# Kernel tuning notes

Measured on AMD Instinct MI355X. Metric: run time of the kernel, lower is better.

## Reference

```python
import jax, jax.numpy as jnp
import numpy as np

B = 64            # number of graphs
N = 2048          # nodes per graph (equal segments; torch.stack in the original requires this)
D = 256           # hidden_dim
G = 4             # num_groups
SUBS = 3          # subclasses per group -> num_classes = 12
C = G * SUBS


def _layer_norm(x, g, b, eps=1e-5):
    mu = jnp.mean(x, axis=-1, keepdims=True)
    var = jnp.var(x, axis=-1, keepdims=True)
    return (x - mu) * jax.lax.rsqrt(var + eps) * g + b


def setup_inputs() -> dict:
    key = jax.random.key(0)
    ks = jax.random.split(key, 20)
    T = B * N
    inp = {
        "node_features": jax.random.normal(ks[0], (T, D), dtype=jnp.float32),
        "batch": jnp.repeat(jnp.arange(B, dtype=jnp.int64), N),  # sorted, equal-size segments
        # group queries (nn.Parameter randn)
        "group_queries": jax.random.normal(ks[1], (G, D), dtype=jnp.float32),
        # per-group projector MLP: D -> 2D -> SUBS*D (stacked over groups)
        "proj_w1": jax.random.normal(ks[2], (G, D, 2 * D), dtype=jnp.float32) * (1.0 / np.sqrt(D)),
        "proj_b1": jnp.zeros((G, 2 * D), dtype=jnp.float32),
        "proj_w2": jax.random.normal(ks[3], (G, 2 * D, SUBS * D), dtype=jnp.float32) * (1.0 / np.sqrt(2 * D)),
        "proj_b2": jnp.zeros((G, SUBS * D), dtype=jnp.float32),
        # output_proj_12: LN -> Linear(D, D//2) -> ReLU -> Linear(D//2, 1)
        "ln12_g": jnp.ones((D,), dtype=jnp.float32),
        "ln12_b": jnp.zeros((D,), dtype=jnp.float32),
        "w12a": jax.random.normal(ks[4], (D, D // 2), dtype=jnp.float32) * (1.0 / np.sqrt(D)),
        "b12a": jnp.zeros((D // 2,), dtype=jnp.float32),
        "w12b": jax.random.normal(ks[5], (D // 2, 1), dtype=jnp.float32) * (1.0 / np.sqrt(D // 2)),
        "b12b": jnp.zeros((1,), dtype=jnp.float32),
        # output_proj_4
        "ln4_g": jnp.ones((D,), dtype=jnp.float32),
        "ln4_b": jnp.zeros((D,), dtype=jnp.float32),
        "w4a": jax.random.normal(ks[6], (D, D // 2), dtype=jnp.float32) * (1.0 / np.sqrt(D)),
        "b4a": jnp.zeros((D // 2,), dtype=jnp.float32),
        "w4b": jax.random.normal(ks[7], (D // 2, 1), dtype=jnp.float32) * (1.0 / np.sqrt(D // 2)),
        "b4b": jnp.zeros((1,), dtype=jnp.float32),
    }
    return inp


def reference(node_features, batch, group_queries, proj_w1, proj_b1, proj_w2, proj_b2,
              ln12_g, ln12_b, w12a, b12a, w12b, b12b,
              ln4_g, ln4_b, w4a, b4a, w4b, b4b):
    # --- derive class queries from group queries (per-group MLP) ---
    h = jax.nn.relu(jnp.einsum('gd,gdh->gh', group_queries, proj_w1) + proj_b1)   # [G, 2D]
    flat = jnp.einsum('gh,ghk->gk', h, proj_w2) + proj_b2                         # [G, SUBS*D]
    # group g maps to global class indices [3g, 3g+1, 3g+2] -> simple reshape gives ordered queries
    class_queries = flat.reshape(C, D)                                            # [12, D]

    scale = jnp.asarray(D ** 0.5, node_features.dtype)
    # equal-size sorted segments: reshape total nodes into [B, N, D] per-graph blocks
    nodes = node_features.reshape(B, N, D)

    # --- 12-class attention pooling ---
    scores12 = jnp.einsum('cd,bnd->bcn', class_queries, nodes) / scale            # [B, 12, N]
    attn12 = jax.nn.softmax(scores12, axis=-1)
    pooled12 = jnp.einsum('bcn,bnd->bcd', attn12, nodes)                          # [B, 12, D]
    x12 = _layer_norm(pooled12, ln12_g, ln12_b)
    logits_12 = (jax.nn.relu(x12 @ w12a + b12a) @ w12b + b12b)[..., 0]            # [B, 12]

    # --- 4-group attention pooling ---
    scores4 = jnp.einsum('gd,bnd->bgn', group_queries, nodes) / scale             # [B, 4, N]
    attn4 = jax.nn.softmax(scores4, axis=-1)
    pooled4 = jnp.einsum('bgn,bnd->bgd', attn4, nodes)                            # [B, 4, D]
    x4 = _layer_norm(pooled4, ln4_g, ln4_b)
    logits_4 = (jax.nn.relu(x4 @ w4a + b4a) @ w4b + b4b)[..., 0]                  # [B, 4]

    return (logits_12, logits_4, attn12)
```

## Files before the change

### kernel.cpp

```cpp
#include <hip/hip_runtime.h>
#include <math.h>

#define BG   64
#define NN   2048
#define DD   256
#define CQ   16
#define NCH  8

static constexpr size_t WS_Q16 = 0;
static constexpr size_t WS_H   = 4096;
static constexpr size_t WS_S   = 6144;
static constexpr size_t WS_ML  = WS_S + (size_t)BG * CQ * NN;
static constexpr size_t WS_PL  = WS_ML + (size_t)BG * NCH * 32;
static constexpr size_t WS_FML = WS_PL + (size_t)BG * NCH * CQ * DD;
static constexpr size_t WS_FIL = WS_FML + 1024;

__global__ __launch_bounds__(256) void kA1(const float* __restrict__ gq,
                                           const float* __restrict__ w1,
                                           const float* __restrict__ b1,
                                           float* __restrict__ ws) {
    int blk = blockIdx.x;
    int g   = blk >> 4;
    int jb  = (blk & 15) * 32;
    int t   = threadIdx.x;
    __shared__ float qlds[256];
    qlds[t] = gq[g * 256 + t];
    if ((blk & 15) == 0) ws[WS_Q16 + (12 + g) * 256 + t] = gq[g * 256 + t];
    __syncthreads();
    int jl = t & 31, dp = t >> 5;
    float acc = 0.f;
    const float* wp = w1 + ((size_t)g * 256) * 512 + jb + jl;
    #pragma unroll 8
    for (int i = 0; i < 32; ++i) {
        int d = dp * 32 + i;
        acc += qlds[d] * wp[(size_t)d * 512];
    }
    __shared__ float red[8][33];
    red[dp][jl] = acc;
    __syncthreads();
    if (dp == 0) {
        float s = 0.f;
        #pragma unroll
        for (int p = 0; p < 8; ++p) s += red[p][jl];
        s += b1[g * 512 + jb + jl];
        ws[WS_H + g * 512 + jb + jl] = fmaxf(s, 0.f);
    }
}

__global__ __launch_bounds__(256) void kA2(const float* __restrict__ w2,
                                           const float* __restrict__ b2,
                                           float* __restrict__ ws) {
    int blk = blockIdx.x;
    int g   = blk / 48;
    int kb  = (blk % 48) * 16;
    int t   = threadIdx.x;
    __shared__ float hlds[512];
    hlds[t]       = ws[WS_H + g * 512 + t];
    hlds[t + 256] = ws[WS_H + g * 512 + t + 256];
    __syncthreads();
    int kl = t & 15, dp = t >> 4;
    float acc = 0.f;
    const float* wp = w2 + ((size_t)g * 512) * 768 + kb + kl;
    #pragma unroll 8
    for (int i = 0; i < 32; ++i) {
        int jj = dp * 32 + i;
        acc += hlds[jj] * wp[(size_t)jj * 768];
    }
    __shared__ float red[16][17];
    red[dp][kl] = acc;
    __syncthreads();
    if (dp == 0) {
        float s = 0.f;
        #pragma unroll
        for (int p = 0; p < 16; ++p) s += red[p][kl];
        ws[WS_Q16 + g * 768 + kb + kl] = s + b2[g * 768 + kb + kl];
    }
}

__global__ __launch_bounds__(256) void kF(const float* __restrict__ x,
                                          float* __restrict__ ws) {
    __shared__ float4 qlds[CQ * 64];
    __shared__ float  wlds[CQ * 256];
    __shared__ float  mbuf[CQ], lbuf[CQ];

    int t   = threadIdx.x;
    int blk = blockIdx.x;
    int b   = blk >> 3, ch = blk & 7;
    int gn0 = b * NN + ch * 256;

    const float4* qg = (const float4*)(ws + WS_Q16);
    #pragma unroll
    for (int i = 0; i < 4; ++i) qlds[t + i * 256] = qg[t + i * 256];
    __syncthreads();

    const float4* xa = (const float4*)x + (size_t)(gn0 + t) * 64;
    float sc[CQ];
    #pragma unroll
    for (int c = 0; c < CQ; ++c) sc[c] = 0.f;

    float4 buf[8];
    #pragma unroll
    for (int i = 0; i < 8; ++i) buf[i] = xa[i];
    for (int base = 0; base < 64; base += 8) {
        float4 cur[8];
        #pragma unroll
        for (int i = 0; i < 8; ++i) cur[i] = buf[i];
        if (base + 8 < 64) {
            #pragma unroll
            for (int i = 0; i < 8; ++i) buf[i] = xa[base + 8 + i];
        }
        #pragma unroll
        for (int i = 0; i < 8; ++i) {
            #pragma unroll
            for (int c = 0; c < CQ; ++c) {
                float4 q = qlds[c * 64 + base + i];
                sc[c] += q.x * cur[i].x + q.y * cur[i].y
                       + q.z * cur[i].z + q.w * cur[i].w;
            }
        }
    }
    #pragma unroll
    for (int c = 0; c < CQ; ++c) sc[c] *= 0.0625f;

    float* srow = ws + WS_S + ((size_t)b * CQ) * NN + ch * 256;
    #pragma unroll
    for (int c = 0; c < CQ; ++c) srow[(size_t)c * NN + t] = sc[c];

    #pragma unroll
    for (int c = 0; c < CQ; ++c) wlds[c * 256 + t] = sc[c];
    __syncthreads();
    {
        int c = t >> 4, slot = t & 15;
        float mv = -1e30f;
        #pragma unroll
        for (int k = 0; k < 16; ++k) mv = fmaxf(mv, wlds[c * 256 + slot + k * 16]);
        #pragma unroll
        for (int off = 1; off < 16; off <<= 1) mv = fmaxf(mv, __shfl_xor(mv, off, 64));
        if (slot == 0) mbuf[c] = mv;
    }
    __syncthreads();
    #pragma unroll
    for (int c = 0; c < CQ; ++c) wlds[c * 256 + t] = __expf(sc[c] - mbuf[c]);
    __syncthreads();
    {
        int c = t >> 4, slot = t & 15;
        float lv = 0.f;
        #pragma unroll
        for (int k = 0; k < 16; ++k) lv += wlds[c * 256 + slot + k * 16];
        #pragma unroll
        for (int off = 1; off < 16; off <<= 1) lv += __shfl_xor(lv, off, 64);
        if (slot == 0) lbuf[c] = lv;
    }
    __syncthreads();
    if (t < CQ) {
        ws[WS_ML + (size_t)blk * 32 + t]      = mbuf[t];
        ws[WS_ML + (size_t)blk * 32 + 16 + t] = lbuf[t];
    }

    int wave = t >> 6, lane = t & 63;
    float4 acc[CQ];
    #pragma unroll
    for (int c = 0; c < CQ; ++c) acc[c] = make_float4(0.f, 0.f, 0.f, 0.f);

    const float4* xq = (const float4*)x + (size_t)(gn0 + wave * 64) * 64 + lane;
    for (int nq = 0; nq < 16; ++nq) {
        float4 x0 = xq[(size_t)(nq * 4 + 0) * 64];
        float4 x1 = xq[(size_t)(nq * 4 + 1) * 64];
        float4 x2 = xq[(size_t)(nq * 4 + 2) * 64];
        float4 x3 = xq[(size_t)(nq * 4 + 3) * 64];
        #pragma unroll
        for (int c = 0; c < CQ; ++c) {
            float4 ev = *(const float4*)&wlds[c * 256 + wave * 64 + nq * 4];
            acc[c].x += ev.x * x0.x + ev.y * x1.x + ev.z * x2.x + ev.w * x3.x;
            acc[c].y += ev.x * x0.y + ev.y * x1.y + ev.z * x2.y + ev.w * x3.y;
            acc[c].z += ev.x * x0.z + ev.y * x1.z + ev.z * x2.z + ev.w * x3.z;
            acc[c].w += ev.x * x0.w + ev.y * x1.w + ev.z * x2.w + ev.w * x3.w;
        }
    }

    float* sdata = (float*)qlds;
    __syncthreads();
    for (int w = 0; w < 4; ++w) {
        if (wave == w) {
            #pragma unroll
            for (int c = 0; c < CQ; ++c) {
                float* dst = &sdata[c * 256 + lane * 4];
                if (w == 0) {
                    dst[0] = acc[c].x; dst[1] = acc[c].y;
                    dst[2] = acc[c].z; dst[3] = acc[c].w;
                } else {
                    dst[0] += acc[c].x; dst[1] += acc[c].y;
                    dst[2] += acc[c].z; dst[3] += acc[c].w;
                }
            }
        }
        __syncthreads();
    }
    float* po = ws + WS_PL + (size_t)blk * (CQ * 256);
    #pragma unroll
    for (int i = 0; i < CQ; ++i) po[t + i * 256] = sdata[t + i * 256];
}

__global__ __launch_bounds__(256) void kE(float* __restrict__ ws,
        const float* __restrict__ lnG12, const float* __restrict__ lnB12,
        const float* __restrict__ wA12,  const float* __restrict__ bA12,
        const float* __restrict__ wB12,  const float* __restrict__ bB12,
        const float* __restrict__ lnG4,  const float* __restrict__ lnB4,
        const float* __restrict__ wA4,   const float* __restrict__ bA4,
        const float* __restrict__ wB4,   const float* __restrict__ bB4,
        float* __restrict__ out) {
    int bc = blockIdx.x;
    int b = bc >> 4, c = bc & 15;
    int t = threadIdx.x, wave = t >> 6, lane = t & 63;

    __shared__ float scl[NCH];
    __shared__ float sinvl;
    if (t == 0) {
        float mi[NCH], li[NCH];
        float m = -1e30f;
        for (int i = 0; i < NCH; ++i) {
            mi[i] = ws[WS_ML + (size_t)(b * NCH + i) * 32 + c];
            li[i] = ws[WS_ML + (size_t)(b * NCH + i) * 32 + 16 + c];
            m = fmaxf(m, mi[i]);
        }
        float l = 0.f;
        for (int i = 0; i < NCH; ++i) {
            float s = __expf(mi[i] - m);
            scl[i] = s;
            l += s * li[i];
        }
        float il = 1.f / l;
        sinvl = il;
        ws[WS_FML + bc] = m;
        ws[WS_FIL + bc] = il;
    }
    __syncthreads();

    float v = 0.f;
    for (int i = 0; i < NCH; ++i)
        v += scl[i] * ws[WS_PL + ((size_t)(b * NCH + i) * CQ + c) * 256 + t];
    v *= sinvl;

    __shared__ float wr1[4], wr2[4];
    float s = v;
    #pragma unroll
    for (int off = 32; off; off >>= 1) s += __shfl_xor(s, off, 64);
    if (lane == 0) wr1[wave] = s;
    __syncthreads();
    float mu = (wr1[0] + wr1[1] + wr1[2] + wr1[3]) * (1.f / 256.f);
    float dv = v - mu;
    s = dv * dv;
    #pragma unroll
    for (int off = 32; off; off >>= 1) s += __shfl_xor(s, off, 64);
    if (lane == 0) wr2[wave] = s;
    __syncthreads();
    float var = (wr2[0] + wr2[1] + wr2[2] + wr2[3]) * (1.f / 256.f);

    bool is12 = (c < 12);
    const float* lg = is12 ? lnG12 : lnG4;
    const float* lb = is12 ? lnB12 : lnB4;
    const float* wA = is12 ? wA12  : wA4;
    const float* bA = is12 ? bA12  : bA4;
    const float* wB = is12 ? wB12  : wB4;
    const float* bB = is12 ? bB12  : bB4;

    __shared__ float ylds[256];
    __shared__ float hred[256];
    __shared__ float hlds[128];
    float y = dv * rsqrtf(var + 1e-5f) * lg[t] + lb[t];
    ylds[t] = y;
    __syncthreads();
    {
        int j = t & 127, half = t >> 7;
        float hh = 0.f;
        const float* wc = wA + (size_t)half * 128 * 128 + j;
        #pragma unroll 4
        for (int d = 0; d < 128; ++d) hh += ylds[half * 128 + d] * wc[(size_t)d * 128];
        hred[t] = hh;
    }
    __syncthreads();
    if (t < 128) hlds[t] = fmaxf(hred[t] + hred[t + 128] + bA[t], 0.f);
    __syncthreads();
    if (t < 64) {
        float pp = hlds[t] * wB[t] + hlds[t + 64] * wB[t + 64];
        #pragma unroll
        for (int off = 32; off; off >>= 1) pp += __shfl_xor(pp, off, 64);
        if (t == 0) {
            float logit = pp + bB[0];
            if (is12) out[b * 12 + c] = logit;
            else      out[768 + b * 4 + (c - 12)] = logit;
        }
    }
}

__global__ __launch_bounds__(256) void kAttn(const float* __restrict__ ws,
                                             float* __restrict__ out_attn) {
    int blk = blockIdx.x;
    int b = blk / 12, c = blk % 12;
    int t = threadIdx.x;
    float m  = ws[WS_FML + b * 16 + c];
    float il = ws[WS_FIL + b * 16 + c];
    const float4* sr = (const float4*)(ws + WS_S + ((size_t)b * CQ + c) * NN);
    float4* ar = (float4*)out_attn + (size_t)(b * 12 + c) * (NN / 4);
    #pragma unroll
    for (int k = 0; k < 2; ++k) {
        float4 v = sr[t + k * 256];
        float4 e;
        e.x = __expf(v.x - m) * il;
        e.y = __expf(v.y - m) * il;
        e.z = __expf(v.z - m) * il;
        e.w = __expf(v.w - m) * il;
        ar[t + k * 256] = e;
    }
}

extern "C" void kernel_launch(void* const* d_in, const int* in_sizes, int n_in,
                              void* d_out, int out_size, void* d_ws, size_t ws_size,
                              hipStream_t stream) {
    const float* x     = (const float*)d_in[0];
    const float* gq    = (const float*)d_in[2];
    const float* w1    = (const float*)d_in[3];
    const float* b1    = (const float*)d_in[4];
    const float* w2    = (const float*)d_in[5];
    const float* b2    = (const float*)d_in[6];
    const float* ln12g = (const float*)d_in[7];
    const float* ln12b = (const float*)d_in[8];
    const float* w12a  = (const float*)d_in[9];
    const float* b12a  = (const float*)d_in[10];
    const float* w12b  = (const float*)d_in[11];
    const float* b12b  = (const float*)d_in[12];
    const float* ln4g  = (const float*)d_in[13];
    const float* ln4b  = (const float*)d_in[14];
    const float* w4a   = (const float*)d_in[15];
    const float* b4a   = (const float*)d_in[16];
    const float* w4b   = (const float*)d_in[17];
    const float* b4b   = (const float*)d_in[18];

    float* out = (float*)d_out;
    float* ws  = (float*)d_ws;

    kA1  <<<64,       256, 0, stream>>>(gq, w1, b1, ws);
    kA2  <<<192,      256, 0, stream>>>(w2, b2, ws);
    kF   <<<BG * NCH, 256, 0, stream>>>(x, ws);
    kE   <<<1024,     256, 0, stream>>>(ws,
            ln12g, ln12b, w12a, b12a, w12b, b12b,
            ln4g,  ln4b,  w4a,  b4a,  w4b,  b4b, out);
    kAttn<<<768,      256, 0, stream>>>(ws, out + 1024);
}
```

Baseline: 289.8 us.

## Halve node chunk per block, split score dot across thread halves, fuse attn write into epilogue

New measurement: 292.8 us. Within noise of the previous version (+1.0%).

```diff
diff --git a/kernel.cpp b/kernel.cpp
--- a/kernel.cpp
+++ b/kernel.cpp
@@ -5,15 +5,14 @@
 #define NN   2048
 #define DD   256
 #define CQ   16
-#define NCH  8
+#define CN   128
+#define NCH  16
 
 static constexpr size_t WS_Q16 = 0;
 static constexpr size_t WS_H   = 4096;
 static constexpr size_t WS_S   = 6144;
 static constexpr size_t WS_ML  = WS_S + (size_t)BG * CQ * NN;
 static constexpr size_t WS_PL  = WS_ML + (size_t)BG * NCH * 32;
-static constexpr size_t WS_FML = WS_PL + (size_t)BG * NCH * CQ * DD;
-static constexpr size_t WS_FIL = WS_FML + 1024;
 
 __global__ __launch_bounds__(256) void kA1(const float* __restrict__ gq,
                                            const float* __restrict__ w1,
@@ -80,20 +79,21 @@
 __global__ __launch_bounds__(256) void kF(const float* __restrict__ x,
                                           float* __restrict__ ws) {
     __shared__ float4 qlds[CQ * 64];
-    __shared__ float  wlds[CQ * 256];
+    __shared__ float  wlds[CQ * CN];
     __shared__ float  mbuf[CQ], lbuf[CQ];
 
     int t   = threadIdx.x;
     int blk = blockIdx.x;
-    int b   = blk >> 3, ch = blk & 7;
-    int gn0 = b * NN + ch * 256;
+    int b   = blk >> 4, ch = blk & 15;
+    int gn0 = b * NN + ch * CN;
 
     const float4* qg = (const float4*)(ws + WS_Q16);
     #pragma unroll
     for (int i = 0; i < 4; ++i) qlds[t + i * 256] = qg[t + i * 256];
     __syncthreads();
 
-    const float4* xa = (const float4*)x + (size_t)(gn0 + t) * 64;
+    int nl = t & 127, half = t >> 7;
+    const float4* xa = (const float4*)x + (size_t)(gn0 + nl) * 64 + half * 32;
     float sc[CQ];
     #pragma unroll
     for (int c = 0; c < CQ; ++c) sc[c] = 0.f;
@@ -101,11 +101,11 @@
     float4 buf[8];
     #pragma unroll
     for (int i = 0; i < 8; ++i) buf[i] = xa[i];
-    for (int base = 0; base < 64; base += 8) {
+    for (int base = 0; base < 32; base += 8) {
         float4 cur[8];
         #pragma unroll
         for (int i = 0; i < 8; ++i) cur[i] = buf[i];
-        if (base + 8 < 64) {
+        if (base + 8 < 32) {
             #pragma unroll
             for (int i = 0; i < 8; ++i) buf[i] = xa[base + 8 + i];
         }
@@ -113,42 +113,50 @@
         for (int i = 0; i < 8; ++i) {
             #pragma unroll
             for (int c = 0; c < CQ; ++c) {
-                float4 q = qlds[c * 64 + base + i];
+                float4 q = qlds[c * 64 + half * 32 + base + i];
                 sc[c] += q.x * cur[i].x + q.y * cur[i].y
                        + q.z * cur[i].z + q.w * cur[i].w;
             }
         }
     }
-    #pragma unroll
-    for (int c = 0; c < CQ; ++c) sc[c] *= 0.0625f;
-
-    float* srow = ws + WS_S + ((size_t)b * CQ) * NN + ch * 256;
-    #pragma unroll
-    for (int c = 0; c < CQ; ++c) srow[(size_t)c * NN + t] = sc[c];
-
-    #pragma unroll
-    for (int c = 0; c < CQ; ++c) wlds[c * 256 + t] = sc[c];
-    __syncthreads();
+    if (half == 1) {
+        #pragma unroll
+        for (int c = 0; c < CQ; ++c) wlds[c * CN + nl] = sc[c];
+    }
+    __syncthreads();
+    if (half == 0) {
+        float* srow = ws + WS_S + ((size_t)b * CQ) * NN + ch * CN;
+        #pragma unroll
+        for (int c = 0; c < CQ; ++c) {
+            float full = (sc[c] + wlds[c * CN + nl]) * 0.0625f;
+            srow[(size_t)c * NN + nl] = full;
+            wlds[c * CN + nl] = full;
+        }
+    }
+    __syncthreads();
+
     {
         int c = t >> 4, slot = t & 15;
         float mv = -1e30f;
         #pragma unroll
-        for (int k = 0; k < 16; ++k) mv = fmaxf(mv, wlds[c * 256 + slot + k * 16]);
-        #pragma unroll
-        for (int off = 1; off < 16; off <<= 1) mv = fmaxf(mv, __shfl_xor(mv, off, 64));
+        for (int k = 0; k < 8; ++k) mv = fmaxf(mv, wlds[c * CN + slot + k * 16]);
+        #pragma unroll
+        for (int off = 8; off; off >>= 1) mv = fmaxf(mv, __shfl_xor(mv, off, 16));
         if (slot == 0) mbuf[c] = mv;
     }
-    __syncthreads();
-    #pragma unroll
-    for (int c = 0; c < CQ; ++c) wlds[c * 256 + t] = __expf(sc[c] - mbuf[c]);
     __syncthreads();
     {
         int c = t >> 4, slot = t & 15;
+        float m = mbuf[c];
         float lv = 0.f;
         #pragma unroll
-        for (int k = 0; k < 16; ++k) lv += wlds[c * 256 + slot + k * 16];
-        #pragma unroll
-        for (int off = 1; off < 16; off <<= 1) lv += __shfl_xor(lv, off, 64);
+        for (int k = 0; k < 8; ++k) {
+            float e = __expf(wlds[c * CN + slot + k * 16] - m);
+            wlds[c * CN + slot + k * 16] = e;
+            lv += e;
+        }
+        #pragma unroll
+        for (int off = 8; off; off >>= 1) lv += __shfl_xor(lv, off, 16);
         if (slot == 0) lbuf[c] = lv;
     }
     __syncthreads();
@@ -162,15 +170,15 @@
     #pragma unroll
     for (int c = 0; c < CQ; ++c) acc[c] = make_float4(0.f, 0.f, 0.f, 0.f);
 
-    const float4* xq = (const float4*)x + (size_t)(gn0 + wave * 64) * 64 + lane;
-    for (int nq = 0; nq < 16; ++nq) {
+    const float4* xq = (const float4*)x + (size_t)(gn0 + wave * 32) * 64 + lane;
+    for (int nq = 0; nq < 8; ++nq) {
         float4 x0 = xq[(size_t)(nq * 4 + 0) * 64];
         float4 x1 = xq[(size_t)(nq * 4 + 1) * 64];
         float4 x2 = xq[(size_t)(nq * 4 + 2) * 64];
         float4 x3 = xq[(size_t)(nq * 4 + 3) * 64];
         #pragma unroll
         for (int c = 0; c < CQ; ++c) {
-            float4 ev = *(const float4*)&wlds[c * 256 + wave * 64 + nq * 4];
+            float4 ev = *(const float4*)&wlds[c * CN + wave * 32 + nq * 4];
             acc[c].x += ev.x * x0.x + ev.y * x1.x + ev.z * x2.x + ev.w * x3.x;
             acc[c].y += ev.x * x0.y + ev.y * x1.y + ev.z * x2.y + ev.w * x3.y;
             acc[c].z += ev.x * x0.z + ev.y * x1.z + ev.z * x2.z + ev.w * x3.z;
@@ -179,7 +187,6 @@
     }
 
     float* sdata = (float*)qlds;
-    __syncthreads();
     for (int w = 0; w < 4; ++w) {
         if (wave == w) {
             #pragma unroll
@@ -208,38 +215,34 @@
         const float* __restrict__ lnG4,  const float* __restrict__ lnB4,
         const float* __restrict__ wA4,   const float* __restrict__ bA4,
         const float* __restrict__ wB4,   const float* __restrict__ bB4,
-        float* __restrict__ out) {
+        float* __restrict__ out, float* __restrict__ out_attn) {
     int bc = blockIdx.x;
     int b = bc >> 4, c = bc & 15;
     int t = threadIdx.x, wave = t >> 6, lane = t & 63;
 
     __shared__ float scl[NCH];
-    __shared__ float sinvl;
-    if (t == 0) {
-        float mi[NCH], li[NCH];
-        float m = -1e30f;
-        for (int i = 0; i < NCH; ++i) {
-            mi[i] = ws[WS_ML + (size_t)(b * NCH + i) * 32 + c];
-            li[i] = ws[WS_ML + (size_t)(b * NCH + i) * 32 + 16 + c];
-            m = fmaxf(m, mi[i]);
-        }
-        float l = 0.f;
-        for (int i = 0; i < NCH; ++i) {
-            float s = __expf(mi[i] - m);
-            scl[i] = s;
-            l += s * li[i];
-        }
-        float il = 1.f / l;
-        sinvl = il;
-        ws[WS_FML + bc] = m;
-        ws[WS_FIL + bc] = il;
-    }
-    __syncthreads();
+    __shared__ float smm, sil;
+    if (t < NCH) {
+        float mi = ws[WS_ML + (size_t)(b * NCH + t) * 32 + c];
+        float li = ws[WS_ML + (size_t)(b * NCH + t) * 32 + 16 + c];
+        float m = mi;
+        #pragma unroll
+        for (int off = 8; off; off >>= 1) m = fmaxf(m, __shfl_xor(m, off, 16));
+        float sc = __expf(mi - m);
+        float ls = sc * li;
+        #pragma unroll
+        for (int off = 8; off; off >>= 1) ls += __shfl_xor(ls, off, 16);
+        scl[t] = sc;
+        if (t == 0) { smm = m; sil = 1.f / ls; }
+    }
+    __syncthreads();
+    float il = sil;
 
     float v = 0.f;
+    #pragma unroll 4
     for (int i = 0; i < NCH; ++i)
         v += scl[i] * ws[WS_PL + ((size_t)(b * NCH + i) * CQ + c) * 256 + t];
-    v *= sinvl;
+    v *= il;
 
     __shared__ float wr1[4], wr2[4];
     float s = v;
@@ -291,26 +294,21 @@
             else      out[768 + b * 4 + (c - 12)] = logit;
         }
     }
-}
-
-__global__ __launch_bounds__(256) void kAttn(const float* __restrict__ ws,
-                                             float* __restrict__ out_attn) {
-    int blk = blockIdx.x;
-    int b = blk / 12, c = blk % 12;
-    int t = threadIdx.x;
-    float m  = ws[WS_FML + b * 16 + c];
-    float il = ws[WS_FIL + b * 16 + c];
-    const float4* sr = (const float4*)(ws + WS_S + ((size_t)b * CQ + c) * NN);
-    float4* ar = (float4*)out_attn + (size_t)(b * 12 + c) * (NN / 4);
-    #pragma unroll
-    for (int k = 0; k < 2; ++k) {
-        float4 v = sr[t + k * 256];
-        float4 e;
-        e.x = __expf(v.x - m) * il;
-        e.y = __expf(v.y - m) * il;
-        e.z = __expf(v.z - m) * il;
-        e.w = __expf(v.w - m) * il;
-        ar[t + k * 256] = e;
+
+    if (is12) {
+        float m = smm;
+        const float4* sr = (const float4*)(ws + WS_S + ((size_t)b * CQ + c) * NN);
+        float4* ar = (float4*)out_attn + (size_t)(b * 12 + c) * (NN / 4);
+        #pragma unroll
+        for (int k = 0; k < 2; ++k) {
+            float4 vv = sr[t + k * 256];
+            float4 e;
+            e.x = __expf(vv.x - m) * il;
+            e.y = __expf(vv.y - m) * il;
+            e.z = __expf(vv.z - m) * il;
+            e.w = __expf(vv.w - m) * il;
+            ar[t + k * 256] = e;
+        }
     }
 }
 
@@ -339,11 +337,10 @@
     float* out = (float*)d_out;
     float* ws  = (float*)d_ws;
 
-    kA1  <<<64,       256, 0, stream>>>(gq, w1, b1, ws);
-    kA2  <<<192,      256, 0, stream>>>(w2, b2, ws);
-    kF   <<<BG * NCH, 256, 0, stream>>>(x, ws);
-    kE   <<<1024,     256, 0, stream>>>(ws,
+    kA1<<<64,       256, 0, stream>>>(gq, w1, b1, ws);
+    kA2<<<192,      256, 0, stream>>>(w2, b2, ws);
+    kF <<<BG * NCH, 256, 0, stream>>>(x, ws);
+    kE <<<1024,     256, 0, stream>>>(ws,
             ln12g, ln12b, w12a, b12a, w12b, b12b,
-            ln4g,  ln4b,  w4a,  b4a,  w4b,  b4b, out);
-    kAttn<<<768,      256, 0, stream>>>(ws, out + 1024);
-}
+            ln4g,  ln4b,  w4a,  b4a,  w4b,  b4b, out, out + 1024);
+}
```
